# Optimization experiments

Measured on AMD Instinct MI355X. Metric: run time of the kernel, lower is better.

## Reference

```python
import jax, jax.numpy as jnp
import numpy as np

HEADS = 16

def rotate_half(x):
    x1, x2 = jnp.split(x, 2, axis=-1)
    return jnp.concatenate((-x2, x1), axis=-1)

def setup_inputs() -> dict:
    key = jax.random.key(0)
    k1, k2, k3, k4 = jax.random.split(key, 4)
    b, n, h = 2, 2048, 1024
    d = h // HEADS
    x = jax.random.normal(k1, (b, n, h), dtype=jnp.float32)
    rotary_emb = jax.random.normal(k2, (n, d), dtype=jnp.float32)
    w_qkv = jax.random.normal(k3, (h, 3 * h), dtype=jnp.float32) * (1.0 / np.sqrt(h))
    w_out = jax.random.normal(k4, (h, h), dtype=jnp.float32) * (1.0 / np.sqrt(h))
    return {"x": x, "rotary_emb": rotary_emb, "w_qkv": w_qkv, "w_out": w_out}

def reference(x, rotary_emb, w_qkv, w_out):
    b, n, hidden = x.shape
    d = hidden // HEADS
    # fused QKV projection: [b,n,3*hidden]
    qkv = jnp.einsum('bnh,hk->bnk', x, w_qkv)
    q, k, v = jnp.split(qkv, 3, axis=-1)
    # [b,n,hidden] -> [b,H,n,d]
    split_heads = lambda t: t.reshape(b, n, HEADS, d).transpose(0, 2, 1, 3)
    q, k, v = split_heads(q), split_heads(k), split_heads(v)
    # rotary: pos is [n,d], broadcast over batch/heads
    cos = jnp.cos(rotary_emb)[None, None]
    sin = jnp.sin(rotary_emb)[None, None]
    q = q * cos + rotate_half(q) * sin
    k = k * cos + rotate_half(k) * sin
    # SDPA (no mask, no dropout)
    scale = 1.0 / np.sqrt(d).astype(np.float32)
    scores = jnp.einsum('bhqd,bhkd->bhqk', q, k) * scale
    attn = jax.nn.softmax(scores, axis=-1)
    out = jnp.einsum('bhqk,bhkd->bhqd', attn, v)
    out = out.transpose(0, 2, 1, 3).reshape(b, n, hidden)
    return jnp.einsum('bnh,hk->bnk', out, w_out)
```

## Files before the change

### kernel.cpp

```cpp
#include <hip/hip_runtime.h>
#include <math.h>

#define HEADS 16
#define DH    64
#define SEQ   2048
#define HID   1024
#define NROW  4096

typedef __attribute__((ext_vector_type(8))) short bf16x8;
typedef __attribute__((ext_vector_type(4))) float f32x4;

#define AS1 __attribute__((address_space(1)))
#define AS3 __attribute__((address_space(3)))

#define QSCALE 0.18033688011112042f

__device__ __forceinline__ unsigned short f2bf(float x) {
    unsigned int u = __builtin_bit_cast(unsigned int, x);
    u = (u + 0x7FFFu + ((u >> 16) & 1u)) >> 16;
    return (unsigned short)u;
}

__device__ __forceinline__ void gload_lds16(const unsigned short* g, unsigned short* l) {
    __builtin_amdgcn_global_load_lds((AS1 void*)g, (AS3 void*)l, 16, 0, 0);
}

__global__ __launch_bounds__(256) void conv_x(const float* __restrict__ x,
                                              unsigned short* __restrict__ xb)
{
    size_t i = ((size_t)blockIdx.x * 256 + threadIdx.x) * 8;
    float4 a = *(const float4*)&x[i];
    float4 b = *(const float4*)&x[i + 4];
    union { unsigned short u[8]; bf16x8 v; } pk;
    pk.u[0] = f2bf(a.x); pk.u[1] = f2bf(a.y); pk.u[2] = f2bf(a.z); pk.u[3] = f2bf(a.w);
    pk.u[4] = f2bf(b.x); pk.u[5] = f2bf(b.y); pk.u[6] = f2bf(b.z); pk.u[7] = f2bf(b.w);
    *(bf16x8*)&xb[i] = pk.v;
}

__global__ __launch_bounds__(256) void rope_tab(const float* __restrict__ rot,
                                                float2* __restrict__ ctab)
{
    int i = blockIdx.x * 256 + threadIdx.x;
    float r = rot[i];
    float s, c;
    __sincosf(r, &s, &c);
    ctab[i] = make_float2(c, s);
}

__global__ __launch_bounds__(256) void wtrans(const float* __restrict__ wsrc,
                                              unsigned short* __restrict__ wt,
                                              int K, int N)
{
    __shared__ float T[64][65];
    const int tid = threadIdx.x;
    const int k0 = blockIdx.y * 64, n0 = blockIdx.x * 64;
    #pragma unroll
    for (int rnd = 0; rnd < 4; ++rnd) {
        int row = (tid >> 4) + rnd * 16;
        int c = (tid & 15) * 4;
        float4 v = *(const float4*)&wsrc[(size_t)(k0 + row) * N + n0 + c];
        T[row][c] = v.x; T[row][c+1] = v.y; T[row][c+2] = v.z; T[row][c+3] = v.w;
    }
    __syncthreads();
    const int sr = tid >> 3, sc = (tid & 7) << 3;
    #pragma unroll
    for (int half = 0; half < 2; ++half) {
        int n = sr + half * 32;
        union { unsigned short u[8]; bf16x8 v; } pk;
        #pragma unroll
        for (int j = 0; j < 8; ++j) pk.u[j] = f2bf(T[sc + j][n]);
        *(bf16x8*)&wt[(size_t)(n0 + n) * K + k0 + sc] = pk.v;
    }
}

__global__ __launch_bounds__(256) void gemm_qkv(const unsigned short* __restrict__ A,
                                                const unsigned short* __restrict__ Bt,
                                                const float2* __restrict__ ctab,
                                                unsigned short* __restrict__ qb,
                                                unsigned short* __restrict__ kb,
                                                unsigned short* __restrict__ vt)
{
    __shared__ __align__(16) unsigned short As[128 * 32];
    __shared__ __align__(16) unsigned short Bs[128 * 32];
    const int tid = threadIdx.x;
    const int w = tid >> 6, lane = tid & 63;
    const int quad = lane >> 4, lm = lane & 15;
    const int wr = (w >> 1) * 64, wc = (w & 1) * 64;
    const int bm = blockIdx.y * 128, bn = blockIdx.x * 128;
    const int m0 = tid >> 2;
    const int sk = (tid & 3) << 3;

    f32x4 acc[4][4];
    #pragma unroll
    for (int i = 0; i < 4; ++i)
        #pragma unroll
        for (int j = 0; j < 4; ++j) acc[i][j] = (f32x4){0.f, 0.f, 0.f, 0.f};

    for (int k0 = 0; k0 < 1024; k0 += 32) {
        __syncthreads();
        gload_lds16(&A [(size_t)(bm + m0     ) * 1024 + k0 + sk], As + (size_t)w * 512);
        gload_lds16(&A [(size_t)(bm + m0 + 64) * 1024 + k0 + sk], As + 2048 + (size_t)w * 512);
        gload_lds16(&Bt[(size_t)(bn + m0     ) * 1024 + k0 + sk], Bs + (size_t)w * 512);
        gload_lds16(&Bt[(size_t)(bn + m0 + 64) * 1024 + k0 + sk], Bs + 2048 + (size_t)w * 512);
        __syncthreads();
        bf16x8 af[4], bfr[4];
        #pragma unroll
        for (int mt = 0; mt < 4; ++mt) af[mt] = *(const bf16x8*)&As[(wr + mt * 16 + lm) * 32 + quad * 8];
        #pragma unroll
        for (int nt = 0; nt < 4; ++nt) bfr[nt] = *(const bf16x8*)&Bs[(wc + nt * 16 + lm) * 32 + quad * 8];
        #pragma unroll
        for (int mt = 0; mt < 4; ++mt)
            #pragma unroll
            for (int nt = 0; nt < 4; ++nt)
                acc[mt][nt] = __builtin_amdgcn_mfma_f32_16x16x32_bf16(af[mt], bfr[nt], acc[mt][nt], 0, 0, 0);
    }

    const int colbase = bn + wc;
    const int region = colbase >> 10;
    const int h = (colbase >> 6) & 15;

    if (region == 2) {
        #pragma unroll
        for (int mt = 0; mt < 4; ++mt) {
            int rowb = bm + wr + mt * 16 + quad * 4;
            int b = rowb >> 11, seq = rowb & (SEQ - 1);
            #pragma unroll
            for (int nt = 0; nt < 4; ++nt) {
                int d = nt * 16 + lm;
                ushort4 pk;
                pk.x = f2bf(acc[mt][nt][0]); pk.y = f2bf(acc[mt][nt][1]);
                pk.z = f2bf(acc[mt][nt][2]); pk.w = f2bf(acc[mt][nt][3]);
                *(ushort4*)&vt[((size_t)(b * HEADS + h) * DH + d) * SEQ + seq] = pk;
            }
        }
    } else {
        const float qs = (region == 0) ? QSCALE : 1.0f;
        unsigned short* dst = (region == 0) ? qb : kb;
        #pragma unroll
        for (int mt = 0; mt < 4; ++mt) {
            #pragma unroll
            for (int nt = 0; nt < 2; ++nt) {
                int d = nt * 16 + lm;
                #pragma unroll
                for (int r = 0; r < 4; ++r) {
                    int row = bm + wr + mt * 16 + quad * 4 + r;
                    int b = row >> 11, seq = row & (SEQ - 1);
                    float2 cs0 = ctab[seq * DH + d];
                    float2 cs1 = ctab[seq * DH + d + 32];
                    float x0 = acc[mt][nt][r];
                    float x1 = acc[mt][nt + 2][r];
                    size_t ob = ((size_t)(b * HEADS + h) * SEQ + seq) * DH;
                    dst[ob + d]      = f2bf((x0 * cs0.x - x1 * cs0.y) * qs);
                    dst[ob + d + 32] = f2bf((x1 * cs1.x + x0 * cs1.y) * qs);
                }
            }
        }
    }
}

#define KVW 72
#define PSW 40
__global__ __launch_bounds__(512, 4) void attn3(const unsigned short* __restrict__ qb,
                                                const unsigned short* __restrict__ kb,
                                                const unsigned short* __restrict__ vt,
                                                unsigned short* __restrict__ attnb)
{
    __shared__ __align__(16) char smem[57344];
    unsigned short* Ks = (unsigned short*)smem;
    unsigned short* Vs = (unsigned short*)(smem + 18432);
    unsigned short* Ps = (unsigned short*)(smem + 36864);

    const int tid = threadIdx.x;
    const int w = tid >> 6, lane = tid & 63, quad = lane >> 4, lm = lane & 15;
    const int g = w >> 2, wq = w & 3;
    const int bh = blockIdx.y, q0 = blockIdx.x * 128;
    const int b = bh >> 4, h = bh & 15;
    const size_t hb = (size_t)bh * SEQ * DH;
    const int sg = tid >> 8;
    const int stid = tid & 255;
    const int sr = stid >> 3, sc = (stid & 7) << 3;
    unsigned short* myPs = Ps + w * (32 * PSW);

    bf16x8 qf[2][2];
    #pragma unroll
    for (int mt = 0; mt < 2; ++mt)
        #pragma unroll
        for (int c = 0; c < 2; ++c)
            qf[mt][c] = *(const bf16x8*)&qb[hb + (size_t)(q0 + wq * 32 + mt * 16 + lm) * DH + c * 32 + quad * 8];

    float rs[2] = {0.f, 0.f};
    f32x4 o[2][4];
    #pragma unroll
    for (int mt = 0; mt < 2; ++mt)
        #pragma unroll
        for (int nt = 0; nt < 4; ++nt) o[mt][nt] = (f32x4){0.f, 0.f, 0.f, 0.f};

    for (int it = 0; it < 16; ++it) {
        const int kbase = sg * 1024 + it * 64;
        __syncthreads();
        *(bf16x8*)&Ks[(sg * 64 + sr     ) * KVW + sc] = *(const bf16x8*)&kb[hb + (size_t)(kbase + sr     ) * DH + sc];
        *(bf16x8*)&Ks[(sg * 64 + sr + 32) * KVW + sc] = *(const bf16x8*)&kb[hb + (size_t)(kbase + sr + 32) * DH + sc];
        *(bf16x8*)&Vs[(sg * 64 + sr     ) * KVW + sc] = *(const bf16x8*)&vt[hb + (size_t)(sr     ) * SEQ + kbase + sc];
        *(bf16x8*)&Vs[(sg * 64 + sr + 32) * KVW + sc] = *(const bf16x8*)&vt[hb + (size_t)(sr + 32) * SEQ + kbase + sc];
        __syncthreads();

        #pragma unroll
        for (int ch = 0; ch < 2; ++ch) {
            f32x4 st[2][2];
            #pragma unroll
            for (int j = 0; j < 2; ++j) {
                const unsigned short* krow = &Ks[(g * 64 + ch * 32 + j * 16 + lm) * KVW];
                bf16x8 a0 = *(const bf16x8*)&krow[quad * 8];
                bf16x8 a1 = *(const bf16x8*)&krow[32 + quad * 8];
                #pragma unroll
                for (int mt = 0; mt < 2; ++mt) {
                    f32x4 z = (f32x4){0.f, 0.f, 0.f, 0.f};
                    z = __builtin_amdgcn_mfma_f32_16x16x32_bf16(a0, qf[mt][0], z, 0, 0, 0);
                    st[mt][j] = __builtin_amdgcn_mfma_f32_16x16x32_bf16(a1, qf[mt][1], st[mt][j] = z, 0, 0, 0);
                }
            }
            #pragma unroll
            for (int mt = 0; mt < 2; ++mt)
                #pragma unroll
                for (int j = 0; j < 2; ++j) {
                    unsigned int u[4];
                    #pragma unroll
                    for (int r = 0; r < 4; ++r) {
                        float p = __builtin_amdgcn_exp2f(st[mt][j][r]);
                        unsigned int pu = __builtin_bit_cast(unsigned int, p) & 0xFFFF0000u;
                        rs[mt] += __builtin_bit_cast(float, pu);
                        u[r] = pu;
                    }
                    unsigned int lo = __builtin_amdgcn_perm(u[1], u[0], 0x07060302);
                    unsigned int hi = __builtin_amdgcn_perm(u[3], u[2], 0x07060302);
                    unsigned long long pv = ((unsigned long long)hi << 32) | lo;
                    *(unsigned long long*)&myPs[(mt * 16 + lm) * PSW + j * 16 + quad * 4] = pv;
                }
            #pragma unroll
            for (int mt = 0; mt < 2; ++mt) {
                bf16x8 pf = *(const bf16x8*)&myPs[(mt * 16 + lm) * PSW + quad * 8];
                #pragma unroll
                for (int nt = 0; nt < 4; ++nt) {
                    bf16x8 vf = *(const bf16x8*)&Vs[(g * 64 + nt * 16 + lm) * KVW + ch * 32 + quad * 8];
                    o[mt][nt] = __builtin_amdgcn_mfma_f32_16x16x32_bf16(pf, vf, o[mt][nt], 0, 0, 0);
                }
            }
        }
    }

    #pragma unroll
    for (int off = 16; off < 64; off <<= 1) {
        rs[0] += __shfl_xor(rs[0], off, 64);
        rs[1] += __shfl_xor(rs[1], off, 64);
    }

    __syncthreads();
    float* mO = (float*)smem;
    float* mL = (float*)(smem + 32768);
    const int mbase = (wq * 64 + lane) * 32;
    if (g == 1) {
        #pragma unroll
        for (int mt = 0; mt < 2; ++mt)
            #pragma unroll
            for (int nt = 0; nt < 4; ++nt)
                *(f32x4*)&mO[mbase + mt * 16 + nt * 4] = o[mt][nt];
        mL[(wq * 64 + lane) * 2 + 0] = rs[0];
        mL[(wq * 64 + lane) * 2 + 1] = rs[1];
    }
    __syncthreads();
    if (g == 0) {
        #pragma unroll
        for (int mt = 0; mt < 2; ++mt)
            #pragma unroll
            for (int nt = 0; nt < 4; ++nt)
                o[mt][nt] += *(const f32x4*)&mO[mbase + mt * 16 + nt * 4];
        rs[0] += mL[(wq * 64 + lane) * 2 + 0];
        rs[1] += mL[(wq * 64 + lane) * 2 + 1];
        #pragma unroll
        for (int mt = 0; mt < 2; ++mt)
            #pragma unroll
            for (int r = 0; r < 4; ++r) {
                float inv = 1.0f / __shfl(rs[mt], quad * 4 + r, 64);
                int row = b * SEQ + q0 + wq * 32 + mt * 16 + quad * 4 + r;
                #pragma unroll
                for (int nt = 0; nt < 4; ++nt)
                    attnb[(size_t)row * HID + h * DH + nt * 16 + lm] = f2bf(o[mt][nt][r] * inv);
            }
    }
}

__global__ __launch_bounds__(256) void gemm_out(const unsigned short* __restrict__ A,
                                                const unsigned short* __restrict__ Bt,
                                                float* __restrict__ C)
{
    __shared__ __align__(16) unsigned short As[128 * 32];
    __shared__ __align__(16) unsigned short Bs[128 * 32];
    const int tid = threadIdx.x;
    const int w = tid >> 6, lane = tid & 63;
    const int quad = lane >> 4, lm = lane & 15;
    const int wr = (w >> 1) * 64, wc = (w & 1) * 64;
    const int bm = blockIdx.y * 128, bn = blockIdx.x * 128;
    const int m0 = tid >> 2;
    const int sk = (tid & 3) << 3;

    f32x4 acc[4][4];
    #pragma unroll
    for (int i = 0; i < 4; ++i)
        #pragma unroll
        for (int j = 0; j < 4; ++j) acc[i][j] = (f32x4){0.f, 0.f, 0.f, 0.f};

    for (int k0 = 0; k0 < 1024; k0 += 32) {
        __syncthreads();
        gload_lds16(&A [(size_t)(bm + m0     ) * 1024 + k0 + sk], As + (size_t)w * 512);
        gload_lds16(&A [(size_t)(bm + m0 + 64) * 1024 + k0 + sk], As + 2048 + (size_t)w * 512);
        gload_lds16(&Bt[(size_t)(bn + m0     ) * 1024 + k0 + sk], Bs + (size_t)w * 512);
        gload_lds16(&Bt[(size_t)(bn + m0 + 64) * 1024 + k0 + sk], Bs + 2048 + (size_t)w * 512);
        __syncthreads();
        bf16x8 af[4], bfr[4];
        #pragma unroll
        for (int mt = 0; mt < 4; ++mt) af[mt] = *(const bf16x8*)&As[(wr + mt * 16 + lm) * 32 + quad * 8];
        #pragma unroll
        for (int nt = 0; nt < 4; ++nt) bfr[nt] = *(const bf16x8*)&Bs[(wc + nt * 16 + lm) * 32 + quad * 8];
        #pragma unroll
        for (int mt = 0; mt < 4; ++mt)
            #pragma unroll
            for (int nt = 0; nt < 4; ++nt)
                acc[mt][nt] = __builtin_amdgcn_mfma_f32_16x16x32_bf16(af[mt], bfr[nt], acc[mt][nt], 0, 0, 0);
    }

    #pragma unroll
    for (int mt = 0; mt < 4; ++mt)
        #pragma unroll
        for (int nt = 0; nt < 4; ++nt) {
            int col = bn + wc + nt * 16 + lm;
            #pragma unroll
            for (int r = 0; r < 4; ++r) {
                int row = bm + wr + mt * 16 + quad * 4 + r;
                C[(size_t)row * 1024 + col] = acc[mt][nt][r];
            }
        }
}

extern "C" void kernel_launch(void* const* d_in, const int* in_sizes, int n_in,
                              void* d_out, int out_size, void* d_ws, size_t ws_size,
                              hipStream_t stream) {
    const float* x     = (const float*)d_in[0];
    const float* rot   = (const float*)d_in[1];
    const float* w_qkv = (const float*)d_in[2];
    const float* w_out = (const float*)d_in[3];
    float* out = (float*)d_out;

    char* ws = (char*)d_ws;
    unsigned short* xb    = (unsigned short*)(ws);
    unsigned short* qb    = (unsigned short*)(ws + (size_t)( 8u << 20));
    unsigned short* kb    = (unsigned short*)(ws + (size_t)(16u << 20));
    unsigned short* vt    = (unsigned short*)(ws + (size_t)(24u << 20));
    unsigned short* attnb = (unsigned short*)(ws + (size_t)(32u << 20));
    unsigned short* wqkvT = (unsigned short*)(ws + (size_t)(40u << 20));
    unsigned short* woutT = (unsigned short*)(ws + (size_t)(46u << 20));
    float2*         ctab  = (float2*)        (ws + (size_t)(48u << 20));

    conv_x<<<2048, 256, 0, stream>>>(x, xb);
    rope_tab<<<512, 256, 0, stream>>>(rot, ctab);
    wtrans<<<dim3(48, 16), 256, 0, stream>>>(w_qkv, wqkvT, 1024, 3072);
    wtrans<<<dim3(16, 16), 256, 0, stream>>>(w_out, woutT, 1024, 1024);

    gemm_qkv<<<dim3(24, 32), 256, 0, stream>>>(xb, wqkvT, ctab, qb, kb, vt);

    attn3<<<dim3(SEQ / 128, 32), 512, 0, stream>>>(qb, kb, vt, attnb);

    gemm_out<<<dim3(8, 32), 256, 0, stream>>>(attnb, woutT, out);
}
```

Measured before the change: 216.3 us.

## Fuse prep kernels, rewrite attention with per-wave key split, shrink out-proj tile

Merges the four preprocessing kernels (x conversion, rope table, two weight transposes) into one launch to cut launch overhead. Rewrites attention so each of four waves covers a 64-query block over its own quarter of the keys, loading K/V fragments straight from global memory into registers instead of staging them through LDS. Partial outputs and row sums are then reduced across waves through shared memory. The output GEMM tile is halved in M to double the block count for better occupancy, at the cost of less B-tile reuse and more redundant global K/V reads.

```diff
diff --git a/kernel.cpp b/kernel.cpp
--- a/kernel.cpp
+++ b/kernel.cpp
@@ -25,35 +25,11 @@
     __builtin_amdgcn_global_load_lds((AS1 void*)g, (AS3 void*)l, 16, 0, 0);
 }
 
-__global__ __launch_bounds__(256) void conv_x(const float* __restrict__ x,
-                                              unsigned short* __restrict__ xb)
-{
-    size_t i = ((size_t)blockIdx.x * 256 + threadIdx.x) * 8;
-    float4 a = *(const float4*)&x[i];
-    float4 b = *(const float4*)&x[i + 4];
-    union { unsigned short u[8]; bf16x8 v; } pk;
-    pk.u[0] = f2bf(a.x); pk.u[1] = f2bf(a.y); pk.u[2] = f2bf(a.z); pk.u[3] = f2bf(a.w);
-    pk.u[4] = f2bf(b.x); pk.u[5] = f2bf(b.y); pk.u[6] = f2bf(b.z); pk.u[7] = f2bf(b.w);
-    *(bf16x8*)&xb[i] = pk.v;
-}
-
-__global__ __launch_bounds__(256) void rope_tab(const float* __restrict__ rot,
-                                                float2* __restrict__ ctab)
-{
-    int i = blockIdx.x * 256 + threadIdx.x;
-    float r = rot[i];
-    float s, c;
-    __sincosf(r, &s, &c);
-    ctab[i] = make_float2(c, s);
-}
-
-__global__ __launch_bounds__(256) void wtrans(const float* __restrict__ wsrc,
-                                              unsigned short* __restrict__ wt,
-                                              int K, int N)
-{
-    __shared__ float T[64][65];
+__device__ void wtrans_body(const float* __restrict__ wsrc, unsigned short* __restrict__ wt,
+                            int K, int N, int bx, int by, float (*T)[65])
+{
     const int tid = threadIdx.x;
-    const int k0 = blockIdx.y * 64, n0 = blockIdx.x * 64;
+    const int k0 = by * 64, n0 = bx * 64;
     #pragma unroll
     for (int rnd = 0; rnd < 4; ++rnd) {
         int row = (tid >> 4) + rnd * 16;
@@ -70,6 +46,40 @@
         #pragma unroll
         for (int j = 0; j < 8; ++j) pk.u[j] = f2bf(T[sc + j][n]);
         *(bf16x8*)&wt[(size_t)(n0 + n) * K + k0 + sc] = pk.v;
+    }
+}
+
+__global__ __launch_bounds__(256) void prep(const float* __restrict__ x,
+                                            const float* __restrict__ rot,
+                                            const float* __restrict__ w_qkv,
+                                            const float* __restrict__ w_out,
+                                            unsigned short* __restrict__ xb,
+                                            float2* __restrict__ ctab,
+                                            unsigned short* __restrict__ wqkvT,
+                                            unsigned short* __restrict__ woutT)
+{
+    __shared__ float T[64][65];
+    const int bid = blockIdx.x;
+    if (bid < 2048) {
+        size_t i = ((size_t)bid * 256 + threadIdx.x) * 8;
+        float4 a = *(const float4*)&x[i];
+        float4 b = *(const float4*)&x[i + 4];
+        union { unsigned short u[8]; bf16x8 v; } pk;
+        pk.u[0] = f2bf(a.x); pk.u[1] = f2bf(a.y); pk.u[2] = f2bf(a.z); pk.u[3] = f2bf(a.w);
+        pk.u[4] = f2bf(b.x); pk.u[5] = f2bf(b.y); pk.u[6] = f2bf(b.z); pk.u[7] = f2bf(b.w);
+        *(bf16x8*)&xb[i] = pk.v;
+    } else if (bid < 2560) {
+        int i = (bid - 2048) * 256 + threadIdx.x;
+        float r = rot[i];
+        float s, c;
+        __sincosf(r, &s, &c);
+        ctab[i] = make_float2(c, s);
+    } else if (bid < 3328) {
+        int idx = bid - 2560;
+        wtrans_body(w_qkv, wqkvT, 1024, 3072, idx % 48, idx / 48, T);
+    } else {
+        int idx = bid - 3328;
+        wtrans_body(w_out, woutT, 1024, 1024, idx % 16, idx / 16, T);
     }
 }
 
@@ -158,133 +168,136 @@
     }
 }
 
-#define KVW 72
-#define PSW 40
-__global__ __launch_bounds__(512, 4) void attn3(const unsigned short* __restrict__ qb,
-                                                const unsigned short* __restrict__ kb,
-                                                const unsigned short* __restrict__ vt,
-                                                unsigned short* __restrict__ attnb)
-{
-    __shared__ __align__(16) char smem[57344];
-    unsigned short* Ks = (unsigned short*)smem;
-    unsigned short* Vs = (unsigned short*)(smem + 18432);
-    unsigned short* Ps = (unsigned short*)(smem + 36864);
+#define PSW 36
+#define OPW 68
+__global__ __launch_bounds__(256) void attn4(const unsigned short* __restrict__ qb,
+                                             const unsigned short* __restrict__ kb,
+                                             const unsigned short* __restrict__ vt,
+                                             unsigned short* __restrict__ attnb)
+{
+    __shared__ __align__(16) char smem[4 * 64 * PSW * 2];
+    unsigned short* Ps   = (unsigned short*)smem;
+    float*          oBuf = (float*)smem;
+    float*          lRed = (float*)(smem + 17408);
 
     const int tid = threadIdx.x;
     const int w = tid >> 6, lane = tid & 63, quad = lane >> 4, lm = lane & 15;
-    const int g = w >> 2, wq = w & 3;
-    const int bh = blockIdx.y, q0 = blockIdx.x * 128;
+    const int bh = blockIdx.y, q0 = blockIdx.x * 64;
     const int b = bh >> 4, h = bh & 15;
     const size_t hb = (size_t)bh * SEQ * DH;
-    const int sg = tid >> 8;
-    const int stid = tid & 255;
-    const int sr = stid >> 3, sc = (stid & 7) << 3;
-    unsigned short* myPs = Ps + w * (32 * PSW);
-
-    bf16x8 qf[2][2];
-    #pragma unroll
-    for (int mt = 0; mt < 2; ++mt)
+    unsigned short* myPs = Ps + w * (64 * PSW);
+
+    bf16x8 qf[4][2];
+    #pragma unroll
+    for (int qt = 0; qt < 4; ++qt)
         #pragma unroll
         for (int c = 0; c < 2; ++c)
-            qf[mt][c] = *(const bf16x8*)&qb[hb + (size_t)(q0 + wq * 32 + mt * 16 + lm) * DH + c * 32 + quad * 8];
-
-    float rs[2] = {0.f, 0.f};
-    f32x4 o[2][4];
-    #pragma unroll
-    for (int mt = 0; mt < 2; ++mt)
-        #pragma unroll
-        for (int nt = 0; nt < 4; ++nt) o[mt][nt] = (f32x4){0.f, 0.f, 0.f, 0.f};
-
+            qf[qt][c] = *(const bf16x8*)&qb[hb + (size_t)(q0 + qt * 16 + lm) * DH + c * 32 + quad * 8];
+
+    float rs[4] = {0.f, 0.f, 0.f, 0.f};
+    f32x4 o[4][4];
+    #pragma unroll
+    for (int qt = 0; qt < 4; ++qt)
+        #pragma unroll
+        for (int dt = 0; dt < 4; ++dt) o[qt][dt] = (f32x4){0.f, 0.f, 0.f, 0.f};
+
+    const int kstart = w * 512;
     for (int it = 0; it < 16; ++it) {
-        const int kbase = sg * 1024 + it * 64;
-        __syncthreads();
-        *(bf16x8*)&Ks[(sg * 64 + sr     ) * KVW + sc] = *(const bf16x8*)&kb[hb + (size_t)(kbase + sr     ) * DH + sc];
-        *(bf16x8*)&Ks[(sg * 64 + sr + 32) * KVW + sc] = *(const bf16x8*)&kb[hb + (size_t)(kbase + sr + 32) * DH + sc];
-        *(bf16x8*)&Vs[(sg * 64 + sr     ) * KVW + sc] = *(const bf16x8*)&vt[hb + (size_t)(sr     ) * SEQ + kbase + sc];
-        *(bf16x8*)&Vs[(sg * 64 + sr + 32) * KVW + sc] = *(const bf16x8*)&vt[hb + (size_t)(sr + 32) * SEQ + kbase + sc];
-        __syncthreads();
-
-        #pragma unroll
-        for (int ch = 0; ch < 2; ++ch) {
-            f32x4 st[2][2];
-            #pragma unroll
-            for (int j = 0; j < 2; ++j) {
-                const unsigned short* krow = &Ks[(g * 64 + ch * 32 + j * 16 + lm) * KVW];
-                bf16x8 a0 = *(const bf16x8*)&krow[quad * 8];
-                bf16x8 a1 = *(const bf16x8*)&krow[32 + quad * 8];
-                #pragma unroll
-                for (int mt = 0; mt < 2; ++mt) {
-                    f32x4 z = (f32x4){0.f, 0.f, 0.f, 0.f};
-                    z = __builtin_amdgcn_mfma_f32_16x16x32_bf16(a0, qf[mt][0], z, 0, 0, 0);
-                    st[mt][j] = __builtin_amdgcn_mfma_f32_16x16x32_bf16(a1, qf[mt][1], st[mt][j] = z, 0, 0, 0);
+        const int kbase = kstart + it * 32;
+        bf16x8 kf[2][2];
+        #pragma unroll
+        for (int kt = 0; kt < 2; ++kt)
+            #pragma unroll
+            for (int c = 0; c < 2; ++c)
+                kf[kt][c] = *(const bf16x8*)&kb[hb + (size_t)(kbase + kt * 16 + lm) * DH + c * 32 + quad * 8];
+        bf16x8 vf[4];
+        #pragma unroll
+        for (int dt = 0; dt < 4; ++dt)
+            vf[dt] = *(const bf16x8*)&vt[hb + (size_t)(dt * 16 + lm) * SEQ + kbase + quad * 8];
+
+        #pragma unroll
+        for (int kt = 0; kt < 2; ++kt) {
+            f32x4 s[4];
+            #pragma unroll
+            for (int qt = 0; qt < 4; ++qt) {
+                f32x4 z = (f32x4){0.f, 0.f, 0.f, 0.f};
+                z = __builtin_amdgcn_mfma_f32_16x16x32_bf16(kf[kt][0], qf[qt][0], z, 0, 0, 0);
+                s[qt] = __builtin_amdgcn_mfma_f32_16x16x32_bf16(kf[kt][1], qf[qt][1], z, 0, 0, 0);
+            }
+            #pragma unroll
+            for (int qt = 0; qt < 4; ++qt) {
+                unsigned int u[4];
+                #pragma unroll
+                for (int r = 0; r < 4; ++r) {
+                    float p = __builtin_amdgcn_exp2f(s[qt][r]);
+                    unsigned int pu = __builtin_bit_cast(unsigned int, p) & 0xFFFF0000u;
+                    rs[qt] += __builtin_bit_cast(float, pu);
+                    u[r] = pu;
                 }
-            }
-            #pragma unroll
-            for (int mt = 0; mt < 2; ++mt)
-                #pragma unroll
-                for (int j = 0; j < 2; ++j) {
-                    unsigned int u[4];
+                unsigned int lo = __builtin_amdgcn_perm(u[1], u[0], 0x07060302);
+                unsigned int hi = __builtin_amdgcn_perm(u[3], u[2], 0x07060302);
+                unsigned long long pv = ((unsigned long long)hi << 32) | lo;
+                *(unsigned long long*)&myPs[(qt * 16 + lm) * PSW + kt * 16 + quad * 4] = pv;
+            }
+        }
+        #pragma unroll
+        for (int qt = 0; qt < 4; ++qt) {
+            bf16x8 pf = *(const bf16x8*)&myPs[(qt * 16 + lm) * PSW + quad * 8];
+            #pragma unroll
+            for (int dt = 0; dt < 4; ++dt)
+                o[qt][dt] = __builtin_amdgcn_mfma_f32_16x16x32_bf16(pf, vf[dt], o[qt][dt], 0, 0, 0);
+        }
+    }
+
+    #pragma unroll
+    for (int off = 16; off < 64; off <<= 1)
+        #pragma unroll
+        for (int qt = 0; qt < 4; ++qt) rs[qt] += __shfl_xor(rs[qt], off, 64);
+
+    __syncthreads();
+    if (w > 0 && quad == 0) {
+        #pragma unroll
+        for (int qt = 0; qt < 4; ++qt) lRed[(w - 1) * 64 + qt * 16 + lm] = rs[qt];
+    }
+    __syncthreads();
+    if (w == 0) {
+        #pragma unroll
+        for (int qt = 0; qt < 4; ++qt)
+            rs[qt] += lRed[qt * 16 + lm] + lRed[64 + qt * 16 + lm] + lRed[128 + qt * 16 + lm];
+    }
+    #pragma unroll
+    for (int s = 1; s < 4; ++s) {
+        __syncthreads();
+        if (w == s) {
+            #pragma unroll
+            for (int qt = 0; qt < 4; ++qt)
+                #pragma unroll
+                for (int dt = 0; dt < 4; ++dt)
                     #pragma unroll
-                    for (int r = 0; r < 4; ++r) {
-                        float p = __builtin_amdgcn_exp2f(st[mt][j][r]);
-                        unsigned int pu = __builtin_bit_cast(unsigned int, p) & 0xFFFF0000u;
-                        rs[mt] += __builtin_bit_cast(float, pu);
-                        u[r] = pu;
-                    }
-                    unsigned int lo = __builtin_amdgcn_perm(u[1], u[0], 0x07060302);
-                    unsigned int hi = __builtin_amdgcn_perm(u[3], u[2], 0x07060302);
-                    unsigned long long pv = ((unsigned long long)hi << 32) | lo;
-                    *(unsigned long long*)&myPs[(mt * 16 + lm) * PSW + j * 16 + quad * 4] = pv;
-                }
-            #pragma unroll
-            for (int mt = 0; mt < 2; ++mt) {
-                bf16x8 pf = *(const bf16x8*)&myPs[(mt * 16 + lm) * PSW + quad * 8];
-                #pragma unroll
-                for (int nt = 0; nt < 4; ++nt) {
-                    bf16x8 vf = *(const bf16x8*)&Vs[(g * 64 + nt * 16 + lm) * KVW + ch * 32 + quad * 8];
-                    o[mt][nt] = __builtin_amdgcn_mfma_f32_16x16x32_bf16(pf, vf, o[mt][nt], 0, 0, 0);
-                }
-            }
-        }
-    }
-
-    #pragma unroll
-    for (int off = 16; off < 64; off <<= 1) {
-        rs[0] += __shfl_xor(rs[0], off, 64);
-        rs[1] += __shfl_xor(rs[1], off, 64);
-    }
-
-    __syncthreads();
-    float* mO = (float*)smem;
-    float* mL = (float*)(smem + 32768);
-    const int mbase = (wq * 64 + lane) * 32;
-    if (g == 1) {
-        #pragma unroll
-        for (int mt = 0; mt < 2; ++mt)
-            #pragma unroll
-            for (int nt = 0; nt < 4; ++nt)
-                *(f32x4*)&mO[mbase + mt * 16 + nt * 4] = o[mt][nt];
-        mL[(wq * 64 + lane) * 2 + 0] = rs[0];
-        mL[(wq * 64 + lane) * 2 + 1] = rs[1];
-    }
-    __syncthreads();
-    if (g == 0) {
-        #pragma unroll
-        for (int mt = 0; mt < 2; ++mt)
-            #pragma unroll
-            for (int nt = 0; nt < 4; ++nt)
-                o[mt][nt] += *(const f32x4*)&mO[mbase + mt * 16 + nt * 4];
-        rs[0] += mL[(wq * 64 + lane) * 2 + 0];
-        rs[1] += mL[(wq * 64 + lane) * 2 + 1];
-        #pragma unroll
-        for (int mt = 0; mt < 2; ++mt)
+                    for (int r = 0; r < 4; ++r)
+                        oBuf[(qt * 16 + quad * 4 + r) * OPW + dt * 16 + lm] = o[qt][dt][r];
+        }
+        __syncthreads();
+        if (w == 0) {
+            #pragma unroll
+            for (int qt = 0; qt < 4; ++qt)
+                #pragma unroll
+                for (int dt = 0; dt < 4; ++dt)
+                    #pragma unroll
+                    for (int r = 0; r < 4; ++r)
+                        o[qt][dt][r] += oBuf[(qt * 16 + quad * 4 + r) * OPW + dt * 16 + lm];
+        }
+    }
+    if (w == 0) {
+        #pragma unroll
+        for (int qt = 0; qt < 4; ++qt)
             #pragma unroll
             for (int r = 0; r < 4; ++r) {
-                float inv = 1.0f / __shfl(rs[mt], quad * 4 + r, 64);
-                int row = b * SEQ + q0 + wq * 32 + mt * 16 + quad * 4 + r;
-                #pragma unroll
-                for (int nt = 0; nt < 4; ++nt)
-                    attnb[(size_t)row * HID + h * DH + nt * 16 + lm] = f2bf(o[mt][nt][r] * inv);
+                float inv = 1.0f / __shfl(rs[qt], quad * 4 + r, 64);
+                int row = b * SEQ + q0 + qt * 16 + quad * 4 + r;
+                #pragma unroll
+                for (int dt = 0; dt < 4; ++dt)
+                    attnb[(size_t)row * HID + h * DH + dt * 16 + lm] = f2bf(o[qt][dt][r] * inv);
             }
     }
 }
@@ -293,43 +306,42 @@
                                                 const unsigned short* __restrict__ Bt,
                                                 float* __restrict__ C)
 {
-    __shared__ __align__(16) unsigned short As[128 * 32];
+    __shared__ __align__(16) unsigned short As[64 * 32];
     __shared__ __align__(16) unsigned short Bs[128 * 32];
     const int tid = threadIdx.x;
     const int w = tid >> 6, lane = tid & 63;
     const int quad = lane >> 4, lm = lane & 15;
-    const int wr = (w >> 1) * 64, wc = (w & 1) * 64;
-    const int bm = blockIdx.y * 128, bn = blockIdx.x * 128;
+    const int wr = (w >> 1) * 32, wc = (w & 1) * 64;
+    const int bm = blockIdx.y * 64, bn = blockIdx.x * 128;
     const int m0 = tid >> 2;
     const int sk = (tid & 3) << 3;
 
-    f32x4 acc[4][4];
-    #pragma unroll
-    for (int i = 0; i < 4; ++i)
+    f32x4 acc[2][4];
+    #pragma unroll
+    for (int i = 0; i < 2; ++i)
         #pragma unroll
         for (int j = 0; j < 4; ++j) acc[i][j] = (f32x4){0.f, 0.f, 0.f, 0.f};
 
     for (int k0 = 0; k0 < 1024; k0 += 32) {
         __syncthreads();
         gload_lds16(&A [(size_t)(bm + m0     ) * 1024 + k0 + sk], As + (size_t)w * 512);
-        gload_lds16(&A [(size_t)(bm + m0 + 64) * 1024 + k0 + sk], As + 2048 + (size_t)w * 512);
         gload_lds16(&Bt[(size_t)(bn + m0     ) * 1024 + k0 + sk], Bs + (size_t)w * 512);
         gload_lds16(&Bt[(size_t)(bn + m0 + 64) * 1024 + k0 + sk], Bs + 2048 + (size_t)w * 512);
         __syncthreads();
-        bf16x8 af[4], bfr[4];
-        #pragma unroll
-        for (int mt = 0; mt < 4; ++mt) af[mt] = *(const bf16x8*)&As[(wr + mt * 16 + lm) * 32 + quad * 8];
+        bf16x8 af[2], bfr[4];
+        #pragma unroll
+        for (int mt = 0; mt < 2; ++mt) af[mt] = *(const bf16x8*)&As[(wr + mt * 16 + lm) * 32 + quad * 8];
         #pragma unroll
         for (int nt = 0; nt < 4; ++nt) bfr[nt] = *(const bf16x8*)&Bs[(wc + nt * 16 + lm) * 32 + quad * 8];
         #pragma unroll
-        for (int mt = 0; mt < 4; ++mt)
+        for (int mt = 0; mt < 2; ++mt)
             #pragma unroll
             for (int nt = 0; nt < 4; ++nt)
                 acc[mt][nt] = __builtin_amdgcn_mfma_f32_16x16x32_bf16(af[mt], bfr[nt], acc[mt][nt], 0, 0, 0);
     }
 
     #pragma unroll
-    for (int mt = 0; mt < 4; ++mt)
+    for (int mt = 0; mt < 2; ++mt)
         #pragma unroll
         for (int nt = 0; nt < 4; ++nt) {
             int col = bn + wc + nt * 16 + lm;
@@ -360,14 +372,11 @@
     unsigned short* woutT = (unsigned short*)(ws + (size_t)(46u << 20));
     float2*         ctab  = (float2*)        (ws + (size_t)(48u << 20));
 
-    conv_x<<<2048, 256, 0, stream>>>(x, xb);
-    rope_tab<<<512, 256, 0, stream>>>(rot, ctab);
-    wtrans<<<dim3(48, 16), 256, 0, stream>>>(w_qkv, wqkvT, 1024, 3072);
-    wtrans<<<dim3(16, 16), 256, 0, stream>>>(w_out, woutT, 1024, 1024);
+    prep<<<3584, 256, 0, stream>>>(x, rot, w_qkv, w_out, xb, ctab, wqkvT, woutT);
 
     gemm_qkv<<<dim3(24, 32), 256, 0, stream>>>(xb, wqkvT, ctab, qb, kb, vt);
 
-    attn3<<<dim3(SEQ / 128, 32), 512, 0, stream>>>(qb, kb, vt, attnb);
-
-    gemm_out<<<dim3(8, 32), 256, 0, stream>>>(attnb, woutT, out);
-}
+    attn4<<<dim3(SEQ / 64, 32), 256, 0, stream>>>(qb, kb, vt, attnb);
+
+    gemm_out<<<dim3(8, 64), 256, 0, stream>>>(attnb, woutT, out);
+}
```

Result: slower. 224.1 us (+3.6%).
